# Kernel tuning notes

Hardware: AMD Instinct MI355X
Metric: run time of the kernel (lower is better)

Reference implementation:

```python
import jax, jax.numpy as jnp
import numpy as np

H_DIM = 1024
N_HEADS = 16
SEQ_LEN = 2048
BATCH = 4


def setup_inputs() -> dict:
    key = jax.random.key(0)
    ks = jax.random.split(key, 9)
    s = 1.0 / np.sqrt(H_DIM)
    return {
        "x": jax.random.normal(ks[0], (BATCH, SEQ_LEN, H_DIM), dtype=jnp.float32),
        "Wq": jax.random.normal(ks[1], (H_DIM, H_DIM), dtype=jnp.float32) * s,
        "bq": jax.random.normal(ks[2], (H_DIM,), dtype=jnp.float32) * 0.01,
        "Wk": jax.random.normal(ks[3], (H_DIM, H_DIM), dtype=jnp.float32) * s,
        "bk": jax.random.normal(ks[4], (H_DIM,), dtype=jnp.float32) * 0.01,
        "Wv": jax.random.normal(ks[5], (H_DIM, H_DIM), dtype=jnp.float32) * s,
        "bv": jax.random.normal(ks[6], (H_DIM,), dtype=jnp.float32) * 0.01,
        "Wo": jax.random.normal(ks[7], (H_DIM, H_DIM), dtype=jnp.float32) * s,
        "bo": jax.random.normal(ks[8], (H_DIM,), dtype=jnp.float32) * 0.01,
    }


def reference(x, Wq, bq, Wk, bk, Wv, bv, Wo, bo):
    B, T, C = x.shape
    N = N_HEADS
    D = C // N
    # projections -> [B, N, T, D]
    def split_heads(t):
        return t.reshape(B, T, N, D).transpose(0, 2, 1, 3)
    q = split_heads(x @ Wq + bq)
    k = split_heads(x @ Wk + bk)
    v = split_heads(x @ Wv + bv)
    scale = 1.0 / jnp.sqrt(jnp.asarray(D, dtype=x.dtype))
    logits = jnp.einsum("bntd,bnsd->bnts", q, k) * scale  # [B,N,T,T]
    causal = jnp.tril(jnp.ones((T, T), dtype=bool))
    logits = jnp.where(causal[None, None], logits, jnp.asarray(-jnp.inf, dtype=x.dtype))
    attn = jax.nn.softmax(logits, axis=-1)
    ctx = jnp.einsum("bnts,bnsd->bntd", attn, v)  # [B,N,T,D]
    ctx = ctx.transpose(0, 2, 1, 3).reshape(B, T, C)
    return ctx @ Wo + bo
```

## Files before the change

kernel.cpp:

```cpp
#include <hip/hip_runtime.h>
#include <hip/hip_bf16.h>


typedef __attribute__((ext_vector_type(8))) short bhalf8;
typedef __attribute__((ext_vector_type(4))) float f32x4;

#define BATCH 4
#define SEQ 2048
#define CDIM 1024
#define NHEAD 16
#define HDIM 64
#define MTOT (BATCH * SEQ)
#define QSCALE 0.18033688011112042f

static __device__ inline unsigned short f2bf(float f) {
    unsigned int u = __float_as_uint(f);
    unsigned int r = (u + 0x7fffu + ((u >> 16) & 1u)) >> 16;
    return (unsigned short)r;
}
static __device__ inline float bf2f(unsigned short u) {
    return __uint_as_float(((unsigned int)u) << 16);
}
static __device__ inline f32x4 zero4() {
    f32x4 z = {0.f, 0.f, 0.f, 0.f};
    return z;
}
static __device__ inline f32x4 MFMA(bhalf8 a, bhalf8 b, f32x4 c) {
    return __builtin_amdgcn_mfma_f32_16x16x32_bf16(a, b, c, 0, 0, 0);
}
static __device__ inline void gload16(const void* g, void* l) {
    __builtin_amdgcn_global_load_lds(
        (const __attribute__((address_space(1))) unsigned int*)g,
        (__attribute__((address_space(3))) unsigned int*)l, 16, 0, 0);
}
static __device__ inline float exp2n(float x) {
    return __builtin_amdgcn_exp2f(x);
}
static __device__ inline unsigned int pkbf16(float lo, float hi) {
    union { __hip_bfloat162 h; unsigned int u; } c;
    c.h = __float22bfloat162_rn(make_float2(lo, hi));
    return c.u;
}

__global__ __launch_bounds__(256) void cast_x_kernel(const float* __restrict__ x,
                                                     short* __restrict__ o, int n8) {
    int i = blockIdx.x * 256 + threadIdx.x;
    if (i >= n8) return;
    const float4* xv = (const float4*)x;
    float4 a = xv[i * 2];
    float4 b = xv[i * 2 + 1];
    bhalf8 r;
    r[0] = (short)f2bf(a.x); r[1] = (short)f2bf(a.y);
    r[2] = (short)f2bf(a.z); r[3] = (short)f2bf(a.w);
    r[4] = (short)f2bf(b.x); r[5] = (short)f2bf(b.y);
    r[6] = (short)f2bf(b.z); r[7] = (short)f2bf(b.w);
    *(bhalf8*)(o + (size_t)i * 8) = r;
}

__global__ __launch_bounds__(256) void wtrans_kernel(const float* __restrict__ W0,
                                                     const float* __restrict__ W1,
                                                     const float* __restrict__ W2,
                                                     const float* __restrict__ W3,
                                                     short* __restrict__ out) {
    __shared__ float t[32][33];
    const float* W = (blockIdx.z == 0) ? W0 : (blockIdx.z == 1) ? W1
                     : (blockIdx.z == 2) ? W2 : W3;
    short* o = out + (size_t)blockIdx.z * CDIM * CDIM;
    int n0 = blockIdx.x * 32, k0 = blockIdx.y * 32;
    int tx = threadIdx.x, ty = threadIdx.y;
    for (int j = 0; j < 4; ++j)
        t[ty + j * 8][tx] = W[(size_t)(k0 + ty + j * 8) * CDIM + n0 + tx];
    __syncthreads();
    for (int j = 0; j < 4; ++j)
        o[(size_t)(n0 + ty + j * 8) * CDIM + k0 + tx] = (short)f2bf(t[tx][ty + j * 8]);
}

template <int MODE, int GN>
__global__ __launch_bounds__(256) void gemm128(const short* __restrict__ A,
                                               const short* __restrict__ Bt,
                                               const float* __restrict__ b0,
                                               const float* __restrict__ b1,
                                               const float* __restrict__ b2,
                                               unsigned short* __restrict__ QKout,
                                               unsigned short* __restrict__ Vout,
                                               float* __restrict__ Fout) {
    __shared__ char lds[32768];
    char* AlB0 = lds;
    char* BlB0 = lds + 16384;

    const int tid = threadIdx.x, lane = tid & 63, w = tid >> 6;
    const int g = lane >> 4, t16 = lane & 15;
    const int wr = w >> 1, wc = w & 1;

    const int f = blockIdx.x;
    const int xcd = f & 7, i = f >> 3;
    const int mt = xcd * 8 + i / GN, nt = i % GN;
    const int tm = mt * 128, tn = nt * 128;
    const int part = tn >> 10;
    const int tnp = tn & 1023;

    const int c0 = tid, c1 = 256 + tid;
    const int r0 = c0 >> 2, r1 = c1 >> 2;
    const int k0c = (c0 & 3) ^ ((r0 >> 1) & 3);
    const int k1c = (c1 & 3) ^ ((r1 >> 1) & 3);
    const short* a0 = A + (size_t)(tm + r0) * 1024 + k0c * 8;
    const short* a1 = A + (size_t)(tm + r1) * 1024 + k1c * 8;
    const short* bp0 = Bt + (size_t)(tn + r0) * 1024 + k0c * 8;
    const short* bp1 = Bt + (size_t)(tn + r1) * 1024 + k1c * 8;

    int aoff[4], boff[4];
#pragma unroll
    for (int mi = 0; mi < 4; ++mi) {
        int row = wr * 64 + mi * 16 + t16;
        aoff[mi] = row * 64 + ((g ^ ((row >> 1) & 3)) << 4);
    }
#pragma unroll
    for (int ni = 0; ni < 4; ++ni) {
        int row = wc * 64 + ni * 16 + t16;
        boff[ni] = row * 64 + ((g ^ ((row >> 1) & 3)) << 4);
    }

    f32x4 acc[4][4];
#pragma unroll
    for (int mi = 0; mi < 4; ++mi)
#pragma unroll
        for (int ni = 0; ni < 4; ++ni) acc[mi][ni] = zero4();

#define STAGE(kt_, bb_)                                                   \
    do {                                                                  \
        int off_ = (kt_) * 32;                                            \
        char* al_ = AlB0 + (bb_) * 8192;                                  \
        char* bl_ = BlB0 + (bb_) * 8192;                                  \
        gload16(a0 + off_, al_ + tid * 16);                               \
        gload16(a1 + off_, al_ + 4096 + tid * 16);                        \
        gload16(bp0 + off_, bl_ + tid * 16);                              \
        gload16(bp1 + off_, bl_ + 4096 + tid * 16);                       \
    } while (0)

    STAGE(0, 0);
    __syncthreads();

#pragma unroll 2
    for (int kt = 0; kt < 32; ++kt) {
        const int buf = kt & 1;
        if (kt + 1 < 32) STAGE(kt + 1, buf ^ 1);
        const char* al = AlB0 + buf * 8192;
        const char* bl = BlB0 + buf * 8192;
        bhalf8 af[4], bfr[4];
#pragma unroll
        for (int mi = 0; mi < 4; ++mi) af[mi] = *(const bhalf8*)(al + aoff[mi]);
#pragma unroll
        for (int ni = 0; ni < 4; ++ni) bfr[ni] = *(const bhalf8*)(bl + boff[ni]);
        __builtin_amdgcn_s_setprio(1);
#pragma unroll
        for (int mi = 0; mi < 4; ++mi)
#pragma unroll
            for (int ni = 0; ni < 4; ++ni)
                acc[mi][ni] = MFMA(af[mi], bfr[ni], acc[mi][ni]);
        __builtin_amdgcn_s_setprio(0);
        __syncthreads();
    }
#undef STAGE

    if (MODE == 0 && part == 2) {
#pragma unroll
        for (int mi = 0; mi < 4; ++mi)
#pragma unroll
            for (int ni = 0; ni < 4; ++ni) {
                int col_l = wc * 64 + ni * 16 + t16;
                float bias = b2[tnp + col_l];
#pragma unroll
                for (int r = 0; r < 4; ++r) {
                    int row_l = wr * 64 + mi * 16 + g * 4 + r;
                    int byte = col_l * 256 + ((row_l * 2) ^ ((col_l & 7) << 4));
                    *(unsigned short*)(lds + byte) = f2bf(acc[mi][ni][r] + bias);
                }
            }
        __syncthreads();
#pragma unroll
        for (int p = 0; p < 8; ++p) {
            int lin = p * 4096 + tid * 16;
            int rv = lin >> 8;
            int inrow = lin & 255;
            int phys = rv * 256 + (inrow ^ ((rv & 7) << 4));
            bhalf8 val = *(const bhalf8*)(lds + phys);
            int n_g = tnp + rv;
            int hh = n_g >> 6, d = n_g & 63;
            int m = tm + (inrow >> 1);
            int bi = m >> 11, t0 = m & 2047;
            *(bhalf8*)(Vout + (((size_t)((bi * NHEAD + hh) * HDIM + d)) << 11) + t0) = val;
        }
    } else {
#pragma unroll
        for (int mi = 0; mi < 4; ++mi)
#pragma unroll
            for (int ni = 0; ni < 4; ++ni) {
                int col_l = wc * 64 + ni * 16 + t16;
                float bias = 0.f;
                if (MODE == 0) bias = (part == 0 ? b0 : b1)[tnp + col_l];
#pragma unroll
                for (int r = 0; r < 4; ++r) {
                    int row_l = wr * 64 + mi * 16 + g * 4 + r;
                    float v = acc[mi][ni][r] + bias;
                    if (MODE == 0 && part == 0) v *= QSCALE;
                    int byte = row_l * 256 + ((col_l * 2) ^ (((row_l >> 2) & 3) << 5));
                    *(unsigned short*)(lds + byte) = f2bf(v);
                }
            }
        __syncthreads();
#pragma unroll
        for (int p = 0; p < 8; ++p) {
            int lin = p * 4096 + tid * 16;
            int row_l = lin >> 8;
            int inrow = lin & 255;
            int phys = row_l * 256 + ((inrow & ~31) ^ (((row_l >> 2) & 3) << 5)) + (inrow & 31);
            bhalf8 val = *(const bhalf8*)(lds + phys);
            int col0 = inrow >> 1;
            int m = tm + row_l;
            if (MODE == 1) {
                int n_g = tn + col0;
                float* op = Fout + (size_t)m * 1024 + n_g;
                float4 o0, o1;
                o0.x = bf2f((unsigned short)val[0]) + b0[n_g + 0];
                o0.y = bf2f((unsigned short)val[1]) + b0[n_g + 1];
                o0.z = bf2f((unsigned short)val[2]) + b0[n_g + 2];
                o0.w = bf2f((unsigned short)val[3]) + b0[n_g + 3];
                o1.x = bf2f((unsigned short)val[4]) + b0[n_g + 4];
                o1.y = bf2f((unsigned short)val[5]) + b0[n_g + 5];
                o1.z = bf2f((unsigned short)val[6]) + b0[n_g + 6];
                o1.w = bf2f((unsigned short)val[7]) + b0[n_g + 7];
                *(float4*)(op) = o0;
                *(float4*)(op + 4) = o1;
            } else {
                int n_g = tnp + col0;
                int bi = m >> 11, t = m & 2047;
                int hh = n_g >> 6, d0 = n_g & 63;
                *(bhalf8*)(QKout +
                           (((size_t)((part * 64 + bi * NHEAD + hh) * SEQ + t)) << 6) + d0) = val;
            }
        }
    }
}

__global__ __launch_bounds__(256) void attn_kernel(const short* __restrict__ Q,
                                                   const short* __restrict__ K,
                                                   const short* __restrict__ V,
                                                   unsigned short* __restrict__ ctx) {
    __shared__ short Kl0[64 * 64];
    __shared__ short Kl1[64 * 64];
    __shared__ short Vl0[64 * 64];
    __shared__ short Vl1[64 * 64];
    __shared__ short Pl[4][16 * 64];

    const int tid = threadIdx.x, lane = tid & 63, w = tid >> 6;
    const int g = lane >> 4, t16 = lane & 15;

    int orig = blockIdx.x;
    int swz = (orig & 7) * 128 + (orig >> 3);
    const int bh = swz >> 4;
    const int sp = swz & 15;

    const short* Qh = Q + ((size_t)bh << 17);
    const short* Kh = K + ((size_t)bh << 17);
    const short* Vh = V + ((size_t)bh << 17);

    int koff[2], voff[2], ldst[2];
#pragma unroll
    for (int it = 0; it < 2; ++it) {
        int c = it * 256 + tid;
        int srow = c >> 3;
        int dc = (c & 7) ^ (srow & 7);
        koff[it] = (srow << 6) + dc * 8;
        voff[it] = (srow << 11) + dc * 8;
        ldst[it] = it * 4096 + w * 1024;
    }

#define STAGE(kv_, KA_, VA_)                                                  \
    do {                                                                      \
        gload16(Kh + koff[0] + ((kv_) << 12), (char*)(KA_) + ldst[0]);        \
        gload16(Kh + koff[1] + ((kv_) << 12), (char*)(KA_) + ldst[1]);        \
        gload16(Vh + voff[0] + ((kv_) << 6), (char*)(VA_) + ldst[0]);         \
        gload16(Vh + voff[1] + ((kv_) << 6), (char*)(VA_) + ldst[1]);         \
    } while (0)

#define TILE(KA_, VA_)                                                        \
    do {                                                                      \
        f32x4 lg[4];                                                          \
        __builtin_amdgcn_s_setprio(1);                                        \
        _Pragma("unroll") for (int cb = 0; cb < 4; ++cb) {                    \
            int s_ = cb * 16 + t16;                                           \
            int sw_ = (s_ & 7) << 4;                                          \
            const char* rowp = (const char*)(KA_) + s_ * 128;                 \
            bhalf8 k0 = *(const bhalf8*)(rowp + ((g * 16) ^ sw_));            \
            bhalf8 k1 = *(const bhalf8*)(rowp + ((64 + g * 16) ^ sw_));       \
            f32x4 z = zero4();                                                \
            z = MFMA(k0, qf0, z);                                             \
            z = MFMA(k1, qf1, z);                                             \
            lg[cb] = z;                                                       \
        }                                                                     \
        __builtin_amdgcn_s_setprio(0);                                        \
        if (kv == qti) {                                                      \
            int rowl = w * 16 + t16;                                          \
            _Pragma("unroll") for (int cb = 0; cb < 4; ++cb) {                \
                int key0 = cb * 16 + g * 4;                                   \
                _Pragma("unroll") for (int r = 0; r < 4; ++r)                 \
                    if (key0 + r > rowl) lg[cb][r] = -1e30f;                  \
            }                                                                 \
        }                                                                     \
        {                                                                     \
            int rowbyte = t16 * 128;                                          \
            _Pragma("unroll") for (int cb = 0; cb < 4; ++cb) {                \
                float e0 = exp2n(lg[cb][0]);                                  \
                float e1 = exp2n(lg[cb][1]);                                  \
                float e2 = exp2n(lg[cb][2]);                                  \
                float e3 = exp2n(lg[cb][3]);                                  \
                uint2 wv;                                                     \
                wv.x = pkbf16(e0, e1);                                        \
                wv.y = pkbf16(e2, e3);                                        \
                int byte = (rowbyte + cb * 32 + g * 8) ^ swb;                 \
                *(uint2*)((char*)Pl[w] + byte) = wv;                          \
            }                                                                 \
        }                                                                     \
        __builtin_amdgcn_s_setprio(1);                                        \
        _Pragma("unroll") for (int kk = 0; kk < 2; ++kk) {                    \
            bhalf8 vf[4];                                                     \
            _Pragma("unroll") for (int db = 0; db < 4; ++db) {                \
                int d = db * 16 + t16;                                        \
                int vbyte = d * 128 + ((kk * 64 + g * 16) ^ ((d & 7) << 4));  \
                vf[db] = *(const bhalf8*)((const char*)(VA_) + vbyte);        \
            }                                                                 \
            int abyte = (t16 * 128 + kk * 64 + g * 16) ^ swb;                 \
            bhalf8 pa = *(const bhalf8*)((const char*)Pl[w] + abyte);         \
            accl = MFMA(pa, ones, accl);                                      \
            _Pragma("unroll") for (int db = 0; db < 4; ++db)                  \
                acc[db] = MFMA(pa, vf[db], acc[db]);                          \
        }                                                                     \
        __builtin_amdgcn_s_setprio(0);                                        \
    } while (0)

    const int b = bh >> 4, hh = bh & 15;
    const int swb = (t16 & 7) << 4;

    bhalf8 ones;
#pragma unroll
    for (int q = 0; q < 8; ++q) ones[q] = (short)0x3F80;

    int buf = 0;
    STAGE(0, Kl0, Vl0);

    for (int ph = 0; ph < 2; ++ph) {
        const int qti = (ph == 0) ? (31 - sp) : sp;
        const int qbase = qti * 64;
        const int ntile = qti + 1;

        bhalf8 qf0, qf1;
        {
            const short* qp = Qh + ((size_t)(qbase + w * 16 + t16) << 6) + g * 8;
            qf0 = *(const bhalf8*)(qp);
            qf1 = *(const bhalf8*)(qp + 32);
        }

        f32x4 acc[4];
        f32x4 accl;
#pragma unroll
        for (int i = 0; i < 4; ++i) acc[i] = zero4();
        accl = zero4();

        __syncthreads();

        for (int kv = 0; kv < ntile; ++kv) {
            bool pre = (kv + 1 < ntile);
            if (buf == 0) {
                if (pre) STAGE(kv + 1, Kl1, Vl1);
                TILE(Kl0, Vl0);
            } else {
                if (pre) STAGE(kv + 1, Kl0, Vl0);
                TILE(Kl1, Vl1);
            }
            __syncthreads();
            buf ^= 1;
        }

        if (ph == 0) {
            if (buf == 0) STAGE(0, Kl0, Vl0);
            else          STAGE(0, Kl1, Vl1);
        }

#pragma unroll
        for (int r = 0; r < 4; ++r) {
            float inv = 1.f / accl[r];
            int t = qbase + w * 16 + g * 4 + r;
            size_t rowoff = (((size_t)(b * SEQ + t)) << 10) + hh * 64;
#pragma unroll
            for (int db = 0; db < 4; ++db)
                ctx[rowoff + db * 16 + t16] = f2bf(acc[db][r] * inv);
        }
    }
#undef TILE
#undef STAGE
}

extern "C" void kernel_launch(void* const* d_in, const int* in_sizes, int n_in,
                              void* d_out, int out_size, void* d_ws, size_t ws_size,
                              hipStream_t stream) {
    const float* x  = (const float*)d_in[0];
    const float* Wq = (const float*)d_in[1];
    const float* bq = (const float*)d_in[2];
    const float* Wk = (const float*)d_in[3];
    const float* bk = (const float*)d_in[4];
    const float* Wv = (const float*)d_in[5];
    const float* bv = (const float*)d_in[6];
    const float* Wo = (const float*)d_in[7];
    const float* bo = (const float*)d_in[8];

    char* ws = (char*)d_ws;
    short* x16 = (short*)(ws);
    short* Wt  = (short*)(ws + (size_t)16 * 1024 * 1024);
    short* Wot = Wt + (size_t)3 * CDIM * CDIM;
    short* Qb  = (short*)(ws + (size_t)24 * 1024 * 1024);
    short* Vb  = (short*)(ws + (size_t)56 * 1024 * 1024);
    short* Ctx = (short*)(ws + (size_t)72 * 1024 * 1024);

    cast_x_kernel<<<dim3(MTOT * CDIM / 8 / 256), dim3(256), 0, stream>>>(
        x, x16, MTOT * CDIM / 8);
    wtrans_kernel<<<dim3(32, 32, 4), dim3(32, 8), 0, stream>>>(Wq, Wk, Wv, Wo, Wt);

    gemm128<0, 24><<<dim3(1536), dim3(256), 0, stream>>>(
        x16, Wt, bq, bk, bv, (unsigned short*)Qb, (unsigned short*)Vb, nullptr);

    attn_kernel<<<dim3(1024), dim3(256), 0, stream>>>(
        Qb, Qb + (size_t)64 * SEQ * HDIM, Vb, (unsigned short*)Ctx);

    gemm128<1, 8><<<dim3(512), dim3(256), 0, stream>>>(
        Ctx, Wot, bo, nullptr, nullptr, nullptr, nullptr, (float*)d_out);
}
```

Baseline: 179.5 us.

## Process both paired query tiles in one pass sharing K/V tile loads

The attention kernel used to handle its two query tiles (31-sp and sp) in two sequential passes, each restaging K/V from global memory into LDS. Now it walks the K/V tiles once for the longer tile. Each staged tile feeds QK^T, softmax and PV for tile A, and also for tile B while kv ≤ qtiB. This removes the duplicate K/V staging and the extra barriers of the second pass, at the cost of higher register pressure from two accumulator sets and a serialized reuse of the per-wave P buffer.

```diff
diff --git a/kernel.cpp b/kernel.cpp
--- a/kernel.cpp
+++ b/kernel.cpp
@@ -283,37 +283,23 @@
         gload16(Vh + voff[1] + ((kv_) << 6), (char*)(VA_) + ldst[1]);         \
     } while (0)
 
-#define TILE(KA_, VA_)                                                        \
+#define SMPV(VA_, lg_, qti_, acc_, accl_)                                     \
     do {                                                                      \
-        f32x4 lg[4];                                                          \
-        __builtin_amdgcn_s_setprio(1);                                        \
-        _Pragma("unroll") for (int cb = 0; cb < 4; ++cb) {                    \
-            int s_ = cb * 16 + t16;                                           \
-            int sw_ = (s_ & 7) << 4;                                          \
-            const char* rowp = (const char*)(KA_) + s_ * 128;                 \
-            bhalf8 k0 = *(const bhalf8*)(rowp + ((g * 16) ^ sw_));            \
-            bhalf8 k1 = *(const bhalf8*)(rowp + ((64 + g * 16) ^ sw_));       \
-            f32x4 z = zero4();                                                \
-            z = MFMA(k0, qf0, z);                                             \
-            z = MFMA(k1, qf1, z);                                             \
-            lg[cb] = z;                                                       \
-        }                                                                     \
-        __builtin_amdgcn_s_setprio(0);                                        \
-        if (kv == qti) {                                                      \
+        if (kv == (qti_)) {                                                   \
             int rowl = w * 16 + t16;                                          \
             _Pragma("unroll") for (int cb = 0; cb < 4; ++cb) {                \
                 int key0 = cb * 16 + g * 4;                                   \
                 _Pragma("unroll") for (int r = 0; r < 4; ++r)                 \
-                    if (key0 + r > rowl) lg[cb][r] = -1e30f;                  \
+                    if (key0 + r > rowl) lg_[cb][r] = -1e30f;                 \
             }                                                                 \
         }                                                                     \
         {                                                                     \
             int rowbyte = t16 * 128;                                          \
             _Pragma("unroll") for (int cb = 0; cb < 4; ++cb) {                \
-                float e0 = exp2n(lg[cb][0]);                                  \
-                float e1 = exp2n(lg[cb][1]);                                  \
-                float e2 = exp2n(lg[cb][2]);                                  \
-                float e3 = exp2n(lg[cb][3]);                                  \
+                float e0 = exp2n(lg_[cb][0]);                                 \
+                float e1 = exp2n(lg_[cb][1]);                                 \
+                float e2 = exp2n(lg_[cb][2]);                                 \
+                float e3 = exp2n(lg_[cb][3]);                                 \
                 uint2 wv;                                                     \
                 wv.x = pkbf16(e0, e1);                                        \
                 wv.y = pkbf16(e2, e3);                                        \
@@ -331,13 +317,32 @@
             }                                                                 \
             int abyte = (t16 * 128 + kk * 64 + g * 16) ^ swb;                 \
             bhalf8 pa = *(const bhalf8*)((const char*)Pl[w] + abyte);         \
-            accl = MFMA(pa, ones, accl);                                      \
+            accl_ = MFMA(pa, ones, accl_);                                    \
             _Pragma("unroll") for (int db = 0; db < 4; ++db)                  \
-                acc[db] = MFMA(pa, vf[db], acc[db]);                          \
+                acc_[db] = MFMA(pa, vf[db], acc_[db]);                        \
         }                                                                     \
         __builtin_amdgcn_s_setprio(0);                                        \
     } while (0)
 
+#define TILE2(KA_, VA_)                                                       \
+    do {                                                                      \
+        bool doB = (kv <= qtiB);                                              \
+        f32x4 lgA[4], lgB[4];                                                 \
+        __builtin_amdgcn_s_setprio(1);                                        \
+        _Pragma("unroll") for (int cb = 0; cb < 4; ++cb) {                    \
+            int s_ = cb * 16 + t16;                                           \
+            int sw_ = (s_ & 7) << 4;                                          \
+            const char* rowp = (const char*)(KA_) + s_ * 128;                 \
+            bhalf8 k0 = *(const bhalf8*)(rowp + ((g * 16) ^ sw_));            \
+            bhalf8 k1 = *(const bhalf8*)(rowp + ((64 + g * 16) ^ sw_));       \
+            lgA[cb] = MFMA(k1, qfA1, MFMA(k0, qfA0, zero4()));                \
+            if (doB) lgB[cb] = MFMA(k1, qfB1, MFMA(k0, qfB0, zero4()));       \
+        }                                                                     \
+        __builtin_amdgcn_s_setprio(0);                                        \
+        SMPV(VA_, lgA, qtiA, accA, acclA);                                    \
+        if (doB) SMPV(VA_, lgB, qtiB, accB, acclB);                           \
+    } while (0)
+
     const int b = bh >> 4, hh = bh & 15;
     const int swb = (t16 & 7) << 4;
 
@@ -345,58 +350,58 @@
 #pragma unroll
     for (int q = 0; q < 8; ++q) ones[q] = (short)0x3F80;
 
+    const int qtiA = 31 - sp, qtiB = sp;
+    const int qbaseA = qtiA * 64, qbaseB = qtiB * 64;
+
+    bhalf8 qfA0, qfA1, qfB0, qfB1;
+    {
+        const short* qpA = Qh + ((size_t)(qbaseA + w * 16 + t16) << 6) + g * 8;
+        qfA0 = *(const bhalf8*)(qpA);
+        qfA1 = *(const bhalf8*)(qpA + 32);
+        const short* qpB = Qh + ((size_t)(qbaseB + w * 16 + t16) << 6) + g * 8;
+        qfB0 = *(const bhalf8*)(qpB);
+        qfB1 = *(const bhalf8*)(qpB + 32);
+    }
+
+    f32x4 accA[4], accB[4], acclA, acclB;
+#pragma unroll
+    for (int i = 0; i < 4; ++i) { accA[i] = zero4(); accB[i] = zero4(); }
+    acclA = zero4();
+    acclB = zero4();
+
     int buf = 0;
     STAGE(0, Kl0, Vl0);
-
-    for (int ph = 0; ph < 2; ++ph) {
-        const int qti = (ph == 0) ? (31 - sp) : sp;
-        const int qbase = qti * 64;
-        const int ntile = qti + 1;
-
-        bhalf8 qf0, qf1;
-        {
-            const short* qp = Qh + ((size_t)(qbase + w * 16 + t16) << 6) + g * 8;
-            qf0 = *(const bhalf8*)(qp);
-            qf1 = *(const bhalf8*)(qp + 32);
+    __syncthreads();
+
+    for (int kv = 0; kv <= qtiA; ++kv) {
+        bool pre = (kv < qtiA);
+        if (buf == 0) {
+            if (pre) STAGE(kv + 1, Kl1, Vl1);
+            TILE2(Kl0, Vl0);
+        } else {
+            if (pre) STAGE(kv + 1, Kl0, Vl0);
+            TILE2(Kl1, Vl1);
         }
-
-        f32x4 acc[4];
-        f32x4 accl;
-#pragma unroll
-        for (int i = 0; i < 4; ++i) acc[i] = zero4();
-        accl = zero4();
-
         __syncthreads();
-
-        for (int kv = 0; kv < ntile; ++kv) {
-            bool pre = (kv + 1 < ntile);
-            if (buf == 0) {
-                if (pre) STAGE(kv + 1, Kl1, Vl1);
-                TILE(Kl0, Vl0);
-            } else {
-                if (pre) STAGE(kv + 1, Kl0, Vl0);
-                TILE(Kl1, Vl1);
-            }
-            __syncthreads();
-            buf ^= 1;
+        buf ^= 1;
+    }
+
+#pragma unroll
+    for (int r = 0; r < 4; ++r) {
+        float invA = 1.f / acclA[r];
+        float invB = 1.f / acclB[r];
+        int tA = qbaseA + w * 16 + g * 4 + r;
+        int tB = qbaseB + w * 16 + g * 4 + r;
+        size_t roA = (((size_t)(b * SEQ + tA)) << 10) + hh * 64;
+        size_t roB = (((size_t)(b * SEQ + tB)) << 10) + hh * 64;
+#pragma unroll
+        for (int db = 0; db < 4; ++db) {
+            ctx[roA + db * 16 + t16] = f2bf(accA[db][r] * invA);
+            ctx[roB + db * 16 + t16] = f2bf(accB[db][r] * invB);
         }
-
-        if (ph == 0) {
-            if (buf == 0) STAGE(0, Kl0, Vl0);
-            else          STAGE(0, Kl1, Vl1);
-        }
-
-#pragma unroll
-        for (int r = 0; r < 4; ++r) {
-            float inv = 1.f / accl[r];
-            int t = qbase + w * 16 + g * 4 + r;
-            size_t rowoff = (((size_t)(b * SEQ + t)) << 10) + hh * 64;
-#pragma unroll
-            for (int db = 0; db < 4; ++db)
-                ctx[rowoff + db * 16 + t16] = f2bf(acc[db][r] * inv);
-        }
-    }
-#undef TILE
+    }
+#undef TILE2
+#undef SMPV
 #undef STAGE
 }
 
```

Result: slower. 186.2 us (+3.7%).
